# Kernel optimization log

Hardware: AMD Instinct MI355X
Metric: run time of the kernel (lower is better)

Reference implementation:

```python
import jax, jax.numpy as jnp
import numpy as np

B, N, C, H = 2, 2048, 256, 16
D = C // H  # head_dim = 16


def _res_linear(x, W, b):
    # ResidualMLP with num_layers=-1 and in_dim==out_dim, input/output residual: x + Linear(x)
    return x + x @ W.T + b


def _split_heads(z):
    # [B, N, H*D] -> [B, H, N, D]
    return z.reshape(B, N, H, D).transpose(0, 2, 1, 3)


def setup_inputs() -> dict:
    key = jax.random.key(0)
    ks = jax.random.split(key, 10)
    def lin(k):
        return 0.02 * jax.random.normal(k, (C, C), dtype=jnp.float32)
    inp = {
        'x': jax.random.normal(ks[0], (B, N, C), dtype=jnp.float32),
        'attention_mask': jnp.ones((B, N), dtype=jnp.float32),
        'Wq1': lin(ks[1]), 'bq1': jnp.zeros((C,), jnp.float32),
        'Wq2': lin(ks[2]), 'bq2': jnp.zeros((C,), jnp.float32),
        'Wq3': lin(ks[3]), 'bq3': jnp.zeros((C,), jnp.float32),
        'Wk1': lin(ks[4]), 'bk1': jnp.zeros((C,), jnp.float32),
        'Wk2': lin(ks[5]), 'bk2': jnp.zeros((C,), jnp.float32),
        'Wk3': lin(ks[6]), 'bk3': jnp.zeros((C,), jnp.float32),
        'Wv': lin(ks[7]), 'bv': jnp.zeros((C,), jnp.float32),
        'Wo': lin(ks[8]), 'bo': jnp.zeros((C,), jnp.float32),
        'gamma': jnp.ones((C,), jnp.float32),
        'beta': jnp.zeros((C,), jnp.float32),
    }
    return inp


def reference(x, attention_mask, Wq1, bq1, Wq2, bq2, Wq3, bq3,
              Wk1, bk1, Wk2, bk2, Wk3, bk3, Wv, bv, Wo, bo, gamma, beta):
    # residual single-linear projections (ResidualMLP num_layers=-1)
    q1 = _split_heads(_res_linear(x, Wq1, bq1))
    q2 = _split_heads(_res_linear(x, Wq2, bq2))
    q3 = _split_heads(_res_linear(x, Wq3, bq3))
    k1 = _split_heads(_res_linear(x, Wk1, bk1))
    k2 = _split_heads(_res_linear(x, Wk2, bk2))
    k3 = _split_heads(_res_linear(x, Wk3, bk3))
    v = _split_heads(_res_linear(x, Wv, bv))
    # kernel = identity; norm_q = norm_k = False
    mask = attention_mask[:, None, :, None]  # [B,1,N,1]
    q1, q2, q3 = q1 * mask, q2 * mask, q3 * mask
    k1, k2, k3, v = k1 * mask, k2 * mask, k3 * mask, v * mask
    scale = jnp.asarray(N, jnp.float32) ** -0.25
    k1, k2, k3, v = k1 * scale, k2 * scale, k3 * scale, v * scale
    # rank-4 state: [B,H,D,D,D,D]
    state = jnp.einsum('bhni,bhnj,bhnk,bhnl->bhijkl', k1, v, k2, k3, optimize=True)
    # contract queries with state: [B,H,N,D]
    out = jnp.einsum('bhni,bhijkl,bhnk,bhnl->bhnj', q1, state, q2, q3, optimize=True)
    out = out.transpose(0, 2, 1, 3).reshape(B, N, C)  # merge heads
    # LayerNorm(channel_dim), eps=1e-5
    mu = jnp.mean(out, axis=-1, keepdims=True)
    var = jnp.mean(jnp.square(out - mu), axis=-1, keepdims=True)
    out = (out - mu) * jax.lax.rsqrt(var + 1e-5) * gamma + beta
    out = out @ Wo.T + bo
    return out
```

## Files before the change

### kernel.cpp

```cpp
#include <hip/hip_runtime.h>
#include <hip/hip_bf16.h>


typedef _Float16 f16;
typedef _Float16 f16x8 __attribute__((ext_vector_type(8)));
typedef _Float16 f16x4 __attribute__((ext_vector_type(4)));
typedef float    f32x16 __attribute__((ext_vector_type(16)));
typedef uint32_t u32x4 __attribute__((ext_vector_type(4)));

#define MFMA32(a, b, c) __builtin_amdgcn_mfma_f32_32x32x16_f16((a), (b), (c), 0, 0, 0)

constexpr size_t OFF_XH  = 0;
constexpr size_t OFF_WH  = 2097152;
constexpr size_t OFF_BSC = 3014656;
constexpr size_t OFF_GH  = 3021824;
constexpr size_t OFF_RSG = 3152896;
constexpr size_t OFF_B2  = 3153920;
constexpr size_t OFF_Y   = 3154944;
constexpr size_t OFF_OPP = 17835008;

struct W7 { const float* W[7]; const float* b[7]; };

__device__ __forceinline__ int toff(int row, int oct) {
    return row * 128 + (((oct) ^ (row & 7)) << 4);
}
__device__ __forceinline__ f16x8 ldfrag(const f16* base, int row, int oct) {
    return *(const f16x8*)((const char*)base + toff(row, oct));
}
__device__ __forceinline__ void stfrag(f16* base, int row, int oct, f16x8 v) {
    *(f16x8*)((char*)base + toff(row, oct)) = v;
}
__device__ __forceinline__ int drow(int reg, int l) {
    return (reg & 3) + ((reg >> 2) << 3) + ((l >> 5) << 2);
}
__device__ __forceinline__ void zero16(f32x16& v) {
#pragma unroll
    for (int i = 0; i < 16; ++i) v[i] = 0.f;
}
__device__ __forceinline__ uint32_t pkrtz(float a, float b) {
    auto h = __builtin_amdgcn_cvt_pkrtz(a, b);
    return __builtin_bit_cast(uint32_t, h);
}
__device__ __forceinline__ void pswap(uint32_t& x, uint32_t& y) {
    asm volatile("v_permlane32_swap_b32 %0, %1" : "+v"(x), "+v"(y));
}

__global__ __launch_bounds__(256) void k_prep(const float* __restrict__ x, W7 p,
                                              float scale,
                                              const float* __restrict__ Wo,
                                              const float* __restrict__ bo,
                                              const float* __restrict__ gamma,
                                              const float* __restrict__ beta,
                                              char* ws) {
    const int bid = blockIdx.x;
    if (bid < 2824) {
        f16* xh  = (f16*)(ws + OFF_XH);
        f16* Wh  = (f16*)(ws + OFF_WH);
        float* bsc = (float*)(ws + OFF_BSC);
        int idx = bid * 256 + threadIdx.x;
        if (idx < 262144) {
            float4 v = ((const float4*)x)[idx];
            f16x4 o; o[0] = (f16)v.x; o[1] = (f16)v.y; o[2] = (f16)v.z; o[3] = (f16)v.w;
            *(f16x4*)(xh + (size_t)idx * 4) = o;
        } else if (idx < 262144 + 458752) {
            int r = idx - 262144;
            int t = r >> 16, cc = r & 65535, c = cc >> 8, k = cc & 255;
            float v = p.W[t][cc] + (c == k ? 1.f : 0.f);
            if (t >= 3) v *= scale;
            Wh[r] = (f16)v;
        } else if (idx < 262144 + 458752 + 1792) {
            int r = idx - 262144 - 458752;
            int t = r >> 8;
            bsc[r] = p.b[t][r & 255] * (t >= 3 ? scale : 1.f);
        }
    } else {
        f16* Gh = (f16*)(ws + OFF_GH);
        float* rsg = (float*)(ws + OFF_RSG);
        float* B2  = (float*)(ws + OFF_B2);
        int c2 = bid - 2824, c = threadIdx.x;
        float wv = Wo[c2 * 256 + c];
        float g = gamma[c] * wv;
        float bb = beta[c] * wv;
        Gh[c2 * 256 + c] = (f16)g;
        __shared__ float sg[4], sb[4];
#pragma unroll
        for (int off = 32; off > 0; off >>= 1) { g += __shfl_down(g, off); bb += __shfl_down(bb, off); }
        if ((c & 63) == 0) { sg[c >> 6] = g; sb[c >> 6] = bb; }
        __syncthreads();
        if (c == 0) {
            rsg[c2] = sg[0] + sg[1] + sg[2] + sg[3];
            B2[c2]  = sb[0] + sb[1] + sb[2] + sb[3] + bo[c2];
        }
    }
}

__global__ __launch_bounds__(512) void k_lin7(const float* __restrict__ mask, char* ws) {
    const f16* xh = (const f16*)(ws + OFF_XH);
    const f16* Wh = (const f16*)(ws + OFF_WH);
    const float* bsc = (const float*)(ws + OFF_BSC);
    f16* Y = (f16*)(ws + OFF_Y);

    const int ct = blockIdx.x;
    const int rt = blockIdx.y;
    const int t = ct >> 1, half = ct & 1;
    const int tid = threadIdx.x, l = tid & 63, w = tid >> 6;
    const int wr = w >> 1, wc = w & 1;

    __shared__ f16 Xl[128 * 64];
    __shared__ f16 Wl[128 * 64];

    f32x16 acc[2];
    zero16(acc[0]); zero16(acc[1]);

    const f16* Wt = Wh + (size_t)t * 65536;
    for (int kt = 0; kt < 4; ++kt) {
        __syncthreads();
#pragma unroll
        for (int e = 0; e < 2; ++e) {
            int g = tid + 512 * e;
            int row = g >> 3, oct = g & 7;
            f16x8 vx = *(const f16x8*)(xh + (size_t)(rt * 128 + row) * 256 + kt * 64 + oct * 8);
            stfrag(Xl, row, oct, vx);
            f16x8 vw = *(const f16x8*)(Wt + (size_t)(half * 128 + row) * 256 + kt * 64 + oct * 8);
            stfrag(Wl, row, oct, vw);
        }
        __syncthreads();
#pragma unroll
        for (int s = 0; s < 4; ++s) {
            int g = s * 2 + (l >> 5);
            f16x8 a0 = ldfrag(Xl, wr * 32 + (l & 31), g);
            f16x8 b0 = ldfrag(Wl, wc * 64 + (l & 31), g);
            f16x8 b1 = ldfrag(Wl, wc * 64 + 32 + (l & 31), g);
            acc[0] = MFMA32(a0, b0, acc[0]);
            acc[1] = MFMA32(a0, b1, acc[1]);
        }
    }

#pragma unroll
    for (int mc = 0; mc < 2; ++mc)
#pragma unroll
        for (int reg = 0; reg < 16; ++reg) {
            int n = rt * 128 + wr * 32 + drow(reg, l);
            int c = half * 128 + wc * 64 + mc * 32 + (l & 31);
            float v = (acc[mc][reg] + bsc[t * 256 + c]) * mask[n];
            Y[(size_t)t * 1048576 + (size_t)n * 256 + c] = (f16)v;
        }
}

__global__ __launch_bounds__(256, 4) void k_attn(char* ws) {
    const f16* Y = (const f16*)(ws + OFF_Y);
    f16* OPP = (f16*)(ws + OFF_OPP);

    const int nt = blockIdx.x;
    const int bh = blockIdx.y;
    const int ms = blockIdx.z;
    const int b = bh >> 4, hb = (bh & 15) * 16;
    const int tid = threadIdx.x, l = tid & 63, w = tid >> 6;
    const int lane31 = l & 31, lhi = l >> 5;
    const int n0 = nt * 128 + w * 32;

    __shared__ f16 kbuf[2][6144];
    __shared__ f16 btb[2][2048];

    f16x8 qf0, qf1, qf2;
    {
        size_t base = ((size_t)(b * 2048 + n0 + lane31)) * 256 + hb + lhi * 8;
        qf0 = *(const f16x8*)(Y + base);
        qf1 = *(const f16x8*)(Y + 1048576 + base);
        qf2 = *(const f16x8*)(Y + 2097152 + base);
    }

    f32x16 acc; zero16(acc);
    f32x16 zzz; zero16(zzz);

    const int klane = lhi * 1024 + lane31 * 8;
    const int jj = lane31 & 15;

    const int km = tid & 127, kdh = tid >> 7;
    const int vm = tid >> 1, vdh = tid & 1;
    const size_t mrow0 = (size_t)(b * 2048 + ms * 1024);
    const f16* Yk0 = Y + (size_t)3 * 1048576 + (mrow0 + km) * 256 + hb + kdh * 8;
    const f16* Yk1 = Yk0 + 1048576;
    const f16* Yk2 = Yk1 + 1048576;
    const f16* Yv  = Y + (size_t)6 * 1048576 + (mrow0 + vm) * 256 + hb + vdh * 8;
    const int kdst = kdh * 1024 + km * 8;

    f16x8 kp0, kp1, kp2, vp;
    kp0 = *(const f16x8*)(Yk0);
    kp1 = *(const f16x8*)(Yk1);
    kp2 = *(const f16x8*)(Yk2);
    vp  = *(const f16x8*)(Yv);
    {
        f16* kb = kbuf[0]; f16* bt = btb[0];
        *(f16x8*)(kb + kdst)        = kp0;
        *(f16x8*)(kb + 2048 + kdst) = kp1;
        *(f16x8*)(kb + 4096 + kdst) = kp2;
#pragma unroll
        for (int e = 0; e < 8; ++e) {
            int j = vdh * 8 + e;
            bt[j * 128 + (((vm >> 3) ^ e) << 3) + (vm & 7)] = vp[e];
        }
    }

    int cur = 0;
    for (int c = 0; c < 8; ++c) {
        __syncthreads();
        if (c < 7) {
            size_t adv = (size_t)(c + 1) * 128 * 256;
            kp0 = *(const f16x8*)(Yk0 + adv);
            kp1 = *(const f16x8*)(Yk1 + adv);
            kp2 = *(const f16x8*)(Yk2 + adv);
            vp  = *(const f16x8*)(Yv + adv);
        }
        const f16* kb = kbuf[cur];
        const f16* bt = btb[cur];
#pragma unroll
        for (int sub = 0; sub < 4; ++sub) {
            f16x8 kf0 = *(const f16x8*)(kb + klane + sub * 256);
            f16x8 kf1 = *(const f16x8*)(kb + klane + 2048 + sub * 256);
            f16x8 kf2 = *(const f16x8*)(kb + klane + 4096 + sub * 256);
            f16x8 bv1 = *(const f16x8*)(bt + jj * 128 + (((sub * 4 + lhi) ^ (jj & 7)) << 3));
            f16x8 bv2 = *(const f16x8*)(bt + jj * 128 + (((sub * 4 + 2 + lhi) ^ (jj & 7)) << 3));
            f32x16 D = MFMA32(kf0, qf0, zzz);
            f32x16 E = MFMA32(kf1, qf1, zzz);
#pragma unroll
            for (int i = 0; i < 16; ++i) D[i] *= E[i];
            E = MFMA32(kf2, qf2, zzz);
#pragma unroll
            for (int i = 0; i < 16; ++i) D[i] *= E[i];
            uint32_t p01 = pkrtz(D[0], D[1]),   p23 = pkrtz(D[2], D[3]);
            uint32_t p45 = pkrtz(D[4], D[5]),   p67 = pkrtz(D[6], D[7]);
            uint32_t p89 = pkrtz(D[8], D[9]),   pAB = pkrtz(D[10], D[11]);
            uint32_t pCD = pkrtz(D[12], D[13]), pEF = pkrtz(D[14], D[15]);
            pswap(p01, p45);
            pswap(p23, p67);
            pswap(p89, pCD);
            pswap(pAB, pEF);
            u32x4 A1 = {p01, p23, p45, p67};
            u32x4 A2 = {p89, pAB, pCD, pEF};
            acc = MFMA32(__builtin_bit_cast(f16x8, A1), bv1, acc);
            acc = MFMA32(__builtin_bit_cast(f16x8, A2), bv2, acc);
        }
        if (c < 7) {
            f16* kb2 = kbuf[cur ^ 1]; f16* bt2 = btb[cur ^ 1];
            *(f16x8*)(kb2 + kdst)        = kp0;
            *(f16x8*)(kb2 + 2048 + kdst) = kp1;
            *(f16x8*)(kb2 + 4096 + kdst) = kp2;
#pragma unroll
            for (int e = 0; e < 8; ++e) {
                int j = vdh * 8 + e;
                bt2[j * 128 + (((vm >> 3) ^ e) << 3) + (vm & 7)] = vp[e];
            }
        }
        cur ^= 1;
    }

    if (lane31 < 16) {
        f16* outp = OPP + (size_t)ms * 1048576;
#pragma unroll
        for (int reg = 0; reg < 16; ++reg) {
            int n = n0 + drow(reg, l);
            outp[((size_t)(b * 2048) + n) * 256 + hb + lane31] = (f16)acc[reg];
        }
    }
}

__global__ __launch_bounds__(256) void k_final(float* __restrict__ out, char* ws) {
    const f16* P0 = (const f16*)(ws + OFF_OPP);
    const f16* P1 = P0 + 1048576;
    const f16* Gh = (const f16*)(ws + OFF_GH);
    const float* rsg = (const float*)(ws + OFF_RSG);
    const float* B2 = (const float*)(ws + OFF_B2);

    const int ct = blockIdx.x;
    const int rt = blockIdx.y;
    const int tid = threadIdx.x, l = tid & 63, w = tid >> 6;
    const int wr = w >> 1, wc = w & 1;

    __shared__ f16 Xl[128 * 64];
    __shared__ f16 Wl[128 * 64];
    __shared__ float muL[128], rsL[128];

    float sum[4] = {0.f, 0.f, 0.f, 0.f}, sumsq[4] = {0.f, 0.f, 0.f, 0.f};

    f32x16 acc[2][2];
#pragma unroll
    for (int m = 0; m < 2; ++m)
#pragma unroll
        for (int mc = 0; mc < 2; ++mc) zero16(acc[m][mc]);

    for (int kt = 0; kt < 4; ++kt) {
        __syncthreads();
#pragma unroll
        for (int e = 0; e < 4; ++e) {
            int g = tid + 256 * e;
            int row = g >> 3, oct = g & 7;
            size_t idx = (size_t)(rt * 128 + row) * 256 + kt * 64 + oct * 8;
            f16x8 va = *(const f16x8*)(P0 + idx);
            f16x8 vb = *(const f16x8*)(P1 + idx);
            f16x8 vx;
#pragma unroll
            for (int q = 0; q < 8; ++q) {
                float f = (float)va[q] + (float)vb[q];
                vx[q] = (f16)f;
                sum[e] += f; sumsq[e] += f * f;
            }
            stfrag(Xl, row, oct, vx);
            f16x8 vw = *(const f16x8*)(Gh + (size_t)(ct * 128 + row) * 256 + kt * 64 + oct * 8);
            stfrag(Wl, row, oct, vw);
        }
        __syncthreads();
#pragma unroll
        for (int s = 0; s < 4; ++s) {
            int g = s * 2 + (l >> 5);
            f16x8 a0 = ldfrag(Xl, wr * 64 + (l & 31), g);
            f16x8 a1 = ldfrag(Xl, wr * 64 + 32 + (l & 31), g);
            f16x8 b0 = ldfrag(Wl, wc * 64 + (l & 31), g);
            f16x8 b1 = ldfrag(Wl, wc * 64 + 32 + (l & 31), g);
            acc[0][0] = MFMA32(a0, b0, acc[0][0]);
            acc[0][1] = MFMA32(a0, b1, acc[0][1]);
            acc[1][0] = MFMA32(a1, b0, acc[1][0]);
            acc[1][1] = MFMA32(a1, b1, acc[1][1]);
        }
    }

#pragma unroll
    for (int e = 0; e < 4; ++e) {
#pragma unroll
        for (int off = 1; off < 8; off <<= 1) {
            sum[e] += __shfl_xor(sum[e], off);
            sumsq[e] += __shfl_xor(sumsq[e], off);
        }
    }
    if ((tid & 7) == 0) {
#pragma unroll
        for (int e = 0; e < 4; ++e) {
            int row = (tid >> 3) + 32 * e;
            float m = sum[e] * (1.f / 256.f);
            float var = sumsq[e] * (1.f / 256.f) - m * m;
            muL[row] = m;
            rsL[row] = rsqrtf(var + 1e-5f);
        }
    }
    __syncthreads();

#pragma unroll
    for (int m = 0; m < 2; ++m)
#pragma unroll
        for (int mc = 0; mc < 2; ++mc)
#pragma unroll
            for (int reg = 0; reg < 16; ++reg) {
                int nloc = wr * 64 + m * 32 + drow(reg, l);
                int n = rt * 128 + nloc;
                int c2 = ct * 128 + wc * 64 + mc * 32 + (l & 31);
                float v = rsL[nloc] * (acc[m][mc][reg] - muL[nloc] * rsg[c2]) + B2[c2];
                out[(size_t)n * 256 + c2] = v;
            }
}

extern "C" void kernel_launch(void* const* d_in, const int* in_sizes, int n_in,
                              void* d_out, int out_size, void* d_ws, size_t ws_size,
                              hipStream_t stream) {
    (void)in_sizes; (void)n_in; (void)out_size; (void)ws_size;
    const float* x    = (const float*)d_in[0];
    const float* mask = (const float*)d_in[1];
    W7 p;
    for (int t = 0; t < 7; ++t) {
        p.W[t] = (const float*)d_in[2 + 2 * t];
        p.b[t] = (const float*)d_in[3 + 2 * t];
    }
    const float* Wo    = (const float*)d_in[16];
    const float* bo    = (const float*)d_in[17];
    const float* gamma = (const float*)d_in[18];
    const float* beta  = (const float*)d_in[19];
    char* ws = (char*)d_ws;

    const float scale = 0.14865088937534013f;

    k_prep <<<3080, 256, 0, stream>>>(x, p, scale, Wo, bo, gamma, beta, ws);
    k_lin7 <<<dim3(14, 32), 512, 0, stream>>>(mask, ws);
    k_attn <<<dim3(16, 32, 2), 256, 0, stream>>>(ws);
    k_final<<<dim3(2, 32), 256, 0, stream>>>((float*)d_out, ws);
}
```

Measured before the change: 69.29 us.

## Write K/V in head-major MFMA-ready layouts and drop LDS staging in attention

New measurement: 72.84 us. 5.1% more time.

```diff
diff --git a/kernel.cpp b/kernel.cpp
--- a/kernel.cpp
+++ b/kernel.cpp
@@ -17,6 +17,8 @@
 constexpr size_t OFF_RSG = 3152896;
 constexpr size_t OFF_B2  = 3153920;
 constexpr size_t OFF_Y   = 3154944;
+constexpr size_t OFF_KH  = 9446400;
+constexpr size_t OFF_VT  = 15737856;
 constexpr size_t OFF_OPP = 17835008;
 
 struct W7 { const float* W[7]; const float* b[7]; };
@@ -98,7 +100,9 @@
     const f16* xh = (const f16*)(ws + OFF_XH);
     const f16* Wh = (const f16*)(ws + OFF_WH);
     const float* bsc = (const float*)(ws + OFF_BSC);
-    f16* Y = (f16*)(ws + OFF_Y);
+    f16* Y  = (f16*)(ws + OFF_Y);
+    f16* Kh = (f16*)(ws + OFF_KH);
+    f16* Vt = (f16*)(ws + OFF_VT);
 
     const int ct = blockIdx.x;
     const int rt = blockIdx.y;
@@ -143,12 +147,24 @@
             int n = rt * 128 + wr * 32 + drow(reg, l);
             int c = half * 128 + wc * 64 + mc * 32 + (l & 31);
             float v = (acc[mc][reg] + bsc[t * 256 + c]) * mask[n];
-            Y[(size_t)t * 1048576 + (size_t)n * 256 + c] = (f16)v;
-        }
-}
-
-__global__ __launch_bounds__(256, 4) void k_attn(char* ws) {
-    const f16* Y = (const f16*)(ws + OFF_Y);
+            f16 hv = (f16)v;
+            if (t < 3) {
+                Y[(size_t)t * 1048576 + (size_t)n * 256 + c] = hv;
+            } else {
+                int bb = n >> 11, m = n & 2047, h16 = c >> 4, d = c & 15;
+                int bhx = bb * 16 + h16;
+                if (t < 6)
+                    Kh[((size_t)(t - 3) * 32 + bhx) * 32768 + m * 16 + d] = hv;
+                else
+                    Vt[(size_t)bhx * 32768 + (m >> 3) * 128 + d * 8 + (m & 7)] = hv;
+            }
+        }
+}
+
+__global__ __launch_bounds__(256) void k_attn(char* ws) {
+    const f16* Y  = (const f16*)(ws + OFF_Y);
+    const f16* Kh = (const f16*)(ws + OFF_KH);
+    const f16* Vt = (const f16*)(ws + OFF_VT);
     f16* OPP = (f16*)(ws + OFF_OPP);
 
     const int nt = blockIdx.x;
@@ -157,75 +173,40 @@
     const int b = bh >> 4, hb = (bh & 15) * 16;
     const int tid = threadIdx.x, l = tid & 63, w = tid >> 6;
     const int lane31 = l & 31, lhi = l >> 5;
-    const int n0 = nt * 128 + w * 32;
-
-    __shared__ f16 kbuf[2][6144];
-    __shared__ f16 btb[2][2048];
-
-    f16x8 qf0, qf1, qf2;
-    {
-        size_t base = ((size_t)(b * 2048 + n0 + lane31)) * 256 + hb + lhi * 8;
-        qf0 = *(const f16x8*)(Y + base);
-        qf1 = *(const f16x8*)(Y + 1048576 + base);
-        qf2 = *(const f16x8*)(Y + 2097152 + base);
-    }
-
-    f32x16 acc; zero16(acc);
+    const int n0 = nt * 256 + w * 64;
+    const int jj = lane31 & 15;
+
+    f16x8 qf[3][2];
+#pragma unroll
+    for (int t = 0; t < 3; ++t)
+#pragma unroll
+        for (int nn = 0; nn < 2; ++nn)
+            qf[t][nn] = *(const f16x8*)(Y + (size_t)t * 1048576 +
+                        ((size_t)(b * 2048 + n0 + nn * 32 + lane31)) * 256 + hb + lhi * 8);
+
+    f32x16 acc[2];
+    zero16(acc[0]); zero16(acc[1]);
     f32x16 zzz; zero16(zzz);
 
-    const int klane = lhi * 1024 + lane31 * 8;
-    const int jj = lane31 & 15;
-
-    const int km = tid & 127, kdh = tid >> 7;
-    const int vm = tid >> 1, vdh = tid & 1;
-    const size_t mrow0 = (size_t)(b * 2048 + ms * 1024);
-    const f16* Yk0 = Y + (size_t)3 * 1048576 + (mrow0 + km) * 256 + hb + kdh * 8;
-    const f16* Yk1 = Yk0 + 1048576;
-    const f16* Yk2 = Yk1 + 1048576;
-    const f16* Yv  = Y + (size_t)6 * 1048576 + (mrow0 + vm) * 256 + hb + vdh * 8;
-    const int kdst = kdh * 1024 + km * 8;
-
-    f16x8 kp0, kp1, kp2, vp;
-    kp0 = *(const f16x8*)(Yk0);
-    kp1 = *(const f16x8*)(Yk1);
-    kp2 = *(const f16x8*)(Yk2);
-    vp  = *(const f16x8*)(Yv);
-    {
-        f16* kb = kbuf[0]; f16* bt = btb[0];
-        *(f16x8*)(kb + kdst)        = kp0;
-        *(f16x8*)(kb + 2048 + kdst) = kp1;
-        *(f16x8*)(kb + 4096 + kdst) = kp2;
-#pragma unroll
-        for (int e = 0; e < 8; ++e) {
-            int j = vdh * 8 + e;
-            bt[j * 128 + (((vm >> 3) ^ e) << 3) + (vm & 7)] = vp[e];
-        }
-    }
-
-    int cur = 0;
-    for (int c = 0; c < 8; ++c) {
-        __syncthreads();
-        if (c < 7) {
-            size_t adv = (size_t)(c + 1) * 128 * 256;
-            kp0 = *(const f16x8*)(Yk0 + adv);
-            kp1 = *(const f16x8*)(Yk1 + adv);
-            kp2 = *(const f16x8*)(Yk2 + adv);
-            vp  = *(const f16x8*)(Yv + adv);
-        }
-        const f16* kb = kbuf[cur];
-        const f16* bt = btb[cur];
-#pragma unroll
-        for (int sub = 0; sub < 4; ++sub) {
-            f16x8 kf0 = *(const f16x8*)(kb + klane + sub * 256);
-            f16x8 kf1 = *(const f16x8*)(kb + klane + 2048 + sub * 256);
-            f16x8 kf2 = *(const f16x8*)(kb + klane + 4096 + sub * 256);
-            f16x8 bv1 = *(const f16x8*)(bt + jj * 128 + (((sub * 4 + lhi) ^ (jj & 7)) << 3));
-            f16x8 bv2 = *(const f16x8*)(bt + jj * 128 + (((sub * 4 + 2 + lhi) ^ (jj & 7)) << 3));
-            f32x16 D = MFMA32(kf0, qf0, zzz);
-            f32x16 E = MFMA32(kf1, qf1, zzz);
+    const f16* Kb0 = Kh + (size_t)bh * 32768 + (ms * 1024 + lane31) * 16 + lhi * 8;
+    const f16* Kb1 = Kb0 + 1048576;
+    const f16* Kb2 = Kb1 + 1048576;
+    const f16* Vb  = Vt + (size_t)bh * 32768 + ms * 16384 + lhi * 128 + jj * 8;
+
+    for (int c = 0; c < 32; ++c) {
+        const int o = c * 512;
+        f16x8 kf0 = *(const f16x8*)(Kb0 + o);
+        f16x8 kf1 = *(const f16x8*)(Kb1 + o);
+        f16x8 kf2 = *(const f16x8*)(Kb2 + o);
+        f16x8 bv1 = *(const f16x8*)(Vb + o);
+        f16x8 bv2 = *(const f16x8*)(Vb + o + 256);
+#pragma unroll
+        for (int nn = 0; nn < 2; ++nn) {
+            f32x16 D = MFMA32(kf0, qf[0][nn], zzz);
+            f32x16 E = MFMA32(kf1, qf[1][nn], zzz);
 #pragma unroll
             for (int i = 0; i < 16; ++i) D[i] *= E[i];
-            E = MFMA32(kf2, qf2, zzz);
+            E = MFMA32(kf2, qf[2][nn], zzz);
 #pragma unroll
             for (int i = 0; i < 16; ++i) D[i] *= E[i];
             uint32_t p01 = pkrtz(D[0], D[1]),   p23 = pkrtz(D[2], D[3]);
@@ -238,30 +219,20 @@
             pswap(pAB, pEF);
             u32x4 A1 = {p01, p23, p45, p67};
             u32x4 A2 = {p89, pAB, pCD, pEF};
-            acc = MFMA32(__builtin_bit_cast(f16x8, A1), bv1, acc);
-            acc = MFMA32(__builtin_bit_cast(f16x8, A2), bv2, acc);
-        }
-        if (c < 7) {
-            f16* kb2 = kbuf[cur ^ 1]; f16* bt2 = btb[cur ^ 1];
-            *(f16x8*)(kb2 + kdst)        = kp0;
-            *(f16x8*)(kb2 + 2048 + kdst) = kp1;
-            *(f16x8*)(kb2 + 4096 + kdst) = kp2;
-#pragma unroll
-            for (int e = 0; e < 8; ++e) {
-                int j = vdh * 8 + e;
-                bt2[j * 128 + (((vm >> 3) ^ e) << 3) + (vm & 7)] = vp[e];
-            }
-        }
-        cur ^= 1;
+            acc[nn] = MFMA32(__builtin_bit_cast(f16x8, A1), bv1, acc[nn]);
+            acc[nn] = MFMA32(__builtin_bit_cast(f16x8, A2), bv2, acc[nn]);
+        }
     }
 
     if (lane31 < 16) {
         f16* outp = OPP + (size_t)ms * 1048576;
 #pragma unroll
-        for (int reg = 0; reg < 16; ++reg) {
-            int n = n0 + drow(reg, l);
-            outp[((size_t)(b * 2048) + n) * 256 + hb + lane31] = (f16)acc[reg];
-        }
+        for (int nn = 0; nn < 2; ++nn)
+#pragma unroll
+            for (int reg = 0; reg < 16; ++reg) {
+                int n = n0 + nn * 32 + drow(reg, l);
+                outp[((size_t)(b * 2048) + n) * 256 + hb + lane31] = (f16)acc[nn][reg];
+            }
     }
 }
 
@@ -379,6 +350,6 @@
 
     k_prep <<<3080, 256, 0, stream>>>(x, p, scale, Wo, bo, gamma, beta, ws);
     k_lin7 <<<dim3(14, 32), 512, 0, stream>>>(mask, ws);
-    k_attn <<<dim3(16, 32, 2), 256, 0, stream>>>(ws);
+    k_attn <<<dim3(8, 32, 2), 256, 0, stream>>>(ws);
     k_final<<<dim3(2, 32), 256, 0, stream>>>((float*)d_out, ws);
 }
```
